# Optimization experiments

Measured on AMD Instinct MI355X. Metric: run time of the kernel, lower is better.

## Reference

```python
import jax, jax.numpy as jnp
import numpy as np

N, E, G, D, L = 10000, 160000, 100, 128, 5
LMAX, SHD, VOCAB = 2, 9, 10
S3 = 3.0 ** 0.5


def _sph(v):
    # e3nn spherical harmonics, normalize=True, normalization='norm' (||Y_l||=1), lmax=2
    r = jnp.linalg.norm(v, axis=-1, keepdims=True)
    u = v / jnp.maximum(r, 1e-12)
    x, y, z = u[:, 0], u[:, 1], u[:, 2]
    y2 = jnp.stack([S3 * x * z, S3 * x * y, y * y - 0.5 * (x * x + z * z), S3 * y * z, 0.5 * S3 * (z * z - x * x)], axis=-1)
    return jnp.concatenate([jnp.ones_like(u[:, :1]), u, y2], axis=-1)  # [E,9]


def _sh_scale(s, w):
    # FullyConnectedTensorProduct(sh, 1x0e, sh): per-l scaling by weight w [.,3]
    return jnp.concatenate([s[:, 0:1] * w[:, 0:1], s[:, 1:4] * w[:, 1:2], s[:, 4:9] * w[:, 2:3]], axis=-1)


def _smean(src, idx, n):
    s = jax.ops.segment_sum(src, idx, num_segments=n)
    c = jax.ops.segment_sum(jnp.ones((src.shape[0], 1), src.dtype), idx, num_segments=n)
    return s / jnp.maximum(c, 1.0)


def _mlp(x, w1, b1, w2, b2, last_act=False):
    h = jax.nn.silu(x @ w1 + b1)
    o = h @ w2 + b2
    return jax.nn.silu(o) if last_act else o


def _forward(atoms, edge_index, batch_ids, pos, emb_table, Wsi1, bsi1, Wsi2, bsi2, WsiC1, bsiC1, WsiC2, bsiC2, Wm1, bm1, Wm2, bm2, Wp1, bp1, Wp2, bp2, Wn1, bn1, Wn2, bn2, Ws1, bs1, Ws2, bs2, Wpred, bpred):
    row, col = edge_index[0], edge_index[1]
    feat = emb_table[atoms]                                  # [N,D]
    # --- SH_INIT ---
    dpos = pos[row] - pos[col]
    dist = jnp.linalg.norm(dpos, axis=-1, keepdims=True)
    msg = _mlp(jnp.concatenate([dist, feat[row], feat[col]], axis=-1), Wsi1, bsi1, Wsi2, bsi2)
    dsh = _sh_scale(jax.lax.stop_gradient(_sph(dpos)), msg)
    sh = _smean(dsh, row, N)                                 # [N,9]
    pos_com = _smean(pos, batch_ids, G)[batch_ids]
    sh = sh + _sh_scale(jax.lax.stop_gradient(_sph(pos - pos_com)), _mlp(feat, WsiC1, bsiC1, WsiC2, bsiC2))
    sh = sh.at[:, :LMAX * LMAX].set(0.0)                     # all_ell=False: keep only highest l
    # --- stacked HEGNN layers via scan ---
    def body(carry, p):
        feat, pos, sh = carry
        wm1, cm1, wm2, cm2, wp1, cp1, wp2, cp2, wn1, cn1, wn2, cn2, ws1, cs1, ws2, cs2 = p
        dp = pos[row] - pos[col]
        d2 = jnp.sum(dp * dp, axis=-1, keepdims=True)        # squared distance
        t = sh[row] * sh[col]
        ip = jnp.concatenate([jnp.sum(t[:, 0:1], -1, keepdims=True), jnp.sum(t[:, 1:4], -1, keepdims=True), jnp.sum(t[:, 4:9], -1, keepdims=True)], axis=-1)
        m = _mlp(jnp.concatenate([feat[row], feat[col], d2, ip], axis=-1), wm1, cm1, wm2, cm2, last_act=True)
        dp = dp * _mlp(m, wp1, cp1, wp2, cp2)
        ds = _sh_scale(sh[row] - sh[col], _mlp(m, ws1, cs1, ws2, cs2))
        m_agg = _smean(m, row, N)
        p_agg = _smean(dp, row, N)
        s_agg = _smean(ds, row, N)
        sh = sh + s_agg
        pos = pos + p_agg
        feat = _mlp(jnp.concatenate([feat, m_agg], axis=-1), wn1, cn1, wn2, cn2)
        return (feat, pos, sh), None
    (feat, pos, sh), _ = jax.lax.scan(body, (feat, pos, sh), (Wm1, bm1, Wm2, bm2, Wp1, bp1, Wp2, bp2, Wn1, bn1, Wn2, bn2, Ws1, bs1, Ws2, bs2))
    # --- equivariant sum-pool + linear pred ---
    pooled = jax.ops.segment_sum(jnp.concatenate([feat, pos, sh], axis=-1), batch_ids, num_segments=G)
    return pooled @ Wpred + bpred                            # [G,1]


def setup_inputs():
    ks = iter(jax.random.split(jax.random.key(0), 48))
    def nrm(shape):
        return jax.random.normal(next(ks), shape, jnp.float32)
    def w(shape):
        return nrm(shape) / np.float32(np.sqrt(shape[-2]))
    z = lambda *s: jnp.zeros(s, jnp.float32)
    inp = dict(
        atoms=jax.random.randint(next(ks), (N,), 0, VOCAB),
        edge_index=jax.random.randint(next(ks), (2, E), 0, N),
        batch_ids=jnp.sort(jax.random.randint(next(ks), (N,), 0, G)),
        pos=nrm((N, 3)),
        emb_table=nrm((VOCAB, D)) * 0.1,
    )
    inp.update(Wsi1=w((2 * D + 1, D)), bsi1=z(D), Wsi2=w((D, LMAX + 1)), bsi2=z(LMAX + 1),
               WsiC1=w((D, D)), bsiC1=z(D), WsiC2=w((D, LMAX + 1)), bsiC2=z(LMAX + 1))
    inp.update(Wm1=w((L, 2 * D + 1 + LMAX + 1, D)), bm1=z(L, D), Wm2=w((L, D, D)), bm2=z(L, D),
               Wp1=w((L, D, D)), bp1=z(L, D), Wp2=w((L, D, 1)), bp2=z(L, 1),
               Wn1=w((L, 2 * D, D)), bn1=z(L, D), Wn2=w((L, D, D)), bn2=z(L, D),
               Ws1=w((L, D, D)), bs1=z(L, D), Ws2=w((L, D, LMAX + 1)), bs2=z(L, LMAX + 1),
               Wpred=w((D + 3 + SHD, 1)), bpred=z(1))
    return inp


def reference(atoms, edge_index, batch_ids, pos, emb_table, Wsi1, bsi1, Wsi2, bsi2, WsiC1, bsiC1, WsiC2, bsiC2, Wm1, bm1, Wm2, bm2, Wp1, bp1, Wp2, bp2, Wn1, bn1, Wn2, bn2, Ws1, bs1, Ws2, bs2, Wpred, bpred):
    return _forward(atoms, edge_index, batch_ids, pos, emb_table, Wsi1, bsi1, Wsi2, bsi2, WsiC1, bsiC1, WsiC2, bsiC2, Wm1, bm1, Wm2, bm2, Wp1, bp1, Wp2, bp2, Wn1, bn1, Wn2, bn2, Ws1, bs1, Ws2, bs2, Wpred, bpred)
```

## Files before the change

kernel.cpp:

```cpp
#include <hip/hip_runtime.h>
#include <math.h>

#define NA 10000
#define NE 160000
#define NG 100
#define DF 128
#define NL 5
#define NAP 10112
#define NSB 40

typedef __attribute__((ext_vector_type(8))) short bfx8;
typedef __attribute__((ext_vector_type(4))) float f32x4;

__device__ __forceinline__ float silu_f(float x) {
    return x / (1.0f + __expf(-x));
}

__device__ __forceinline__ unsigned short f2bf(float x) {
    unsigned u = __builtin_bit_cast(unsigned, x);
    u = (u + 0x7FFFu + ((u >> 16) & 1u)) >> 16;
    return (unsigned short)u;
}
__device__ __forceinline__ float bf2f(unsigned short h) {
    unsigned u = ((unsigned)h) << 16;
    return __builtin_bit_cast(float, u);
}
__device__ __forceinline__ unsigned packbf(float lo, float hi) {
    return (unsigned)f2bf(lo) | ((unsigned)f2bf(hi) << 16);
}

__device__ __forceinline__ void sph9(float dx, float dy, float dz, float* s) {
    float r = sqrtf(dx * dx + dy * dy + dz * dz);
    float inv = 1.0f / fmaxf(r, 1e-12f);
    float x = dx * inv, y = dy * inv, z = dz * inv;
    const float S3 = 1.7320508075688772f;
    s[0] = 1.0f;
    s[1] = x; s[2] = y; s[3] = z;
    s[4] = S3 * x * z;
    s[5] = S3 * x * y;
    s[6] = y * y - 0.5f * (x * x + z * z);
    s[7] = S3 * y * z;
    s[8] = 0.5f * S3 * (z * z - x * x);
}

#define OFF_SI1   0
#define OFF_SIC1  36864
#define LBASE     53248
#define LSIZE     135168
#define LOFF_M1   0
#define LOFF_M2   36864
#define LOFF_P1   53248
#define LOFF_S1   69632
#define LOFF_N1   86016
#define LOFF_N2   118784
#define WT_TOTAL  729088

__global__ void k_prep_w(const float* __restrict__ Wsi1, const float* __restrict__ WsiC1,
                         const float* __restrict__ Wm1, const float* __restrict__ Wm2,
                         const float* __restrict__ Wp1, const float* __restrict__ Ws1,
                         const float* __restrict__ Wn1, const float* __restrict__ Wn2,
                         unsigned short* __restrict__ WT) {
    int flat = blockIdx.x * 256 + threadIdx.x;
    if (flat >= WT_TOTAL) return;
    float v = 0.0f;
    if (flat < OFF_SIC1) {
        int o = flat - OFF_SI1;
        int n = o / 288, k = o % 288;
        if (k < 256)       v = Wsi1[(k + 1) * 128 + n];
        else if (k == 256) v = Wsi1[n];
    } else if (flat < LBASE) {
        int o = flat - OFF_SIC1;
        int n = o / 128, k = o % 128;
        v = WsiC1[k * 128 + n];
    } else {
        int t = flat - LBASE;
        int lyr = t / LSIZE;
        int o = t % LSIZE;
        if (o < LOFF_M2) {
            int n = o / 288, k = o % 288;
            if (k < 260) v = Wm1[(size_t)lyr * 260 * 128 + k * 128 + n];
        } else if (o < LOFF_P1) {
            int o2 = o - LOFF_M2; int n = o2 / 128, k = o2 % 128;
            v = Wm2[(size_t)lyr * 16384 + k * 128 + n];
        } else if (o < LOFF_S1) {
            int o2 = o - LOFF_P1; int n = o2 / 128, k = o2 % 128;
            v = Wp1[(size_t)lyr * 16384 + k * 128 + n];
        } else if (o < LOFF_N1) {
            int o2 = o - LOFF_S1; int n = o2 / 128, k = o2 % 128;
            v = Ws1[(size_t)lyr * 16384 + k * 128 + n];
        } else if (o < LOFF_N2) {
            int o2 = o - LOFF_N1; int n = o2 / 256, k = o2 % 256;
            v = Wn1[(size_t)lyr * 32768 + k * 128 + n];
        } else {
            int o2 = o - LOFF_N2; int n = o2 / 128, k = o2 % 128;
            v = Wn2[(size_t)lyr * 16384 + k * 128 + n];
        }
    }
    WT[flat] = f2bf(v);
}

template <int KP, int MODE, bool ACT, int NOUT, bool F32OUT>
__global__ __launch_bounds__(256) void gemm_mfma(
    const unsigned short* __restrict__ Ab,
    const unsigned short* __restrict__ WT,
    const float* __restrict__ bias,
    unsigned short* __restrict__ Cb, float* __restrict__ Cf, int M,
    const int* __restrict__ rowI, const int* __restrict__ colI,
    const unsigned short* __restrict__ featb, const unsigned short* __restrict__ tailb,
    const float* __restrict__ W2, const float* __restrict__ b2,
    float* __restrict__ outS)
{
    constexpr int NO = (NOUT > 0) ? NOUT : 1;
    __shared__ unsigned short As[128 * 40];
    __shared__ unsigned short Bs[128 * 40];
    __shared__ float W2s[128 * NO];
    __shared__ float sacc[128 * NO];

    const int tid = threadIdx.x;
    const int m0 = blockIdx.x * 128;
    const int mlo = tid >> 2;
    const int part = tid & 3;

    if (NOUT > 0) {
        for (int t = tid; t < 128 * NO; t += 256) {
            W2s[t] = W2[t];
            sacc[t] = 0.0f;
        }
    }

    int er0 = 0, ec0 = 0, er1 = 0, ec1 = 0;
    if (MODE == 1) {
        er0 = rowI[m0 + mlo];      ec0 = colI[m0 + mlo];
        er1 = rowI[m0 + mlo + 64]; ec1 = colI[m0 + mlo + 64];
    }

    const int w = tid >> 6;
    const int l = tid & 63;
    const int quad = l >> 4;
    const int lm = l & 15;
    const int wm = (w >> 1) * 64, wn = (w & 1) * 64;

    float bv[4];
#pragma unroll
    for (int j = 0; j < 4; j++) bv[j] = bias[wn + j * 16 + lm];

    f32x4 acc[4][4] = {};

    constexpr int NCH = KP / 32;
#pragma unroll 1
    for (int c = 0; c < NCH; c++) {
        const int k0 = c * 32;
#pragma unroll
        for (int i = 0; i < 2; i++) {
            const int m = mlo + i * 64;
            uint4 v;
            if (MODE == 0) {
                v = *(const uint4*)(Ab + (size_t)(m0 + m) * KP + k0 + part * 8);
            } else {
                if (k0 < 128) {
                    int e = i ? er1 : er0;
                    v = *(const uint4*)(featb + (size_t)e * 128 + k0 + part * 8);
                } else if (k0 < 256) {
                    int e = i ? ec1 : ec0;
                    v = *(const uint4*)(featb + (size_t)e * 128 + (k0 - 128) + part * 8);
                } else {
                    if (part == 0) v = *(const uint4*)(tailb + (size_t)(m0 + m) * 16);
                    else           v = make_uint4(0, 0, 0, 0);
                }
            }
            *(uint4*)&As[m * 40 + part * 8] = v;
            uint4 wv = *(const uint4*)(WT + (size_t)m * KP + k0 + part * 8);
            *(uint4*)&Bs[m * 40 + part * 8] = wv;
        }
        __syncthreads();
        bfx8 a[4], b[4];
#pragma unroll
        for (int i = 0; i < 4; i++) a[i] = *(const bfx8*)&As[(wm + i * 16 + lm) * 40 + quad * 8];
#pragma unroll
        for (int j = 0; j < 4; j++) b[j] = *(const bfx8*)&Bs[(wn + j * 16 + lm) * 40 + quad * 8];
#pragma unroll
        for (int i = 0; i < 4; i++)
#pragma unroll
            for (int j = 0; j < 4; j++)
                acc[i][j] = __builtin_amdgcn_mfma_f32_16x16x32_bf16(a[i], b[j], acc[i][j], 0, 0, 0);
        __syncthreads();
    }

    if (NOUT > 0) {
#pragma unroll
        for (int i = 0; i < 4; i++) {
#pragma unroll
            for (int r = 0; r < 4; r++) {
                const int rowL = wm + i * 16 + quad * 4 + r;
                float ps[NO];
#pragma unroll
                for (int o = 0; o < NO; o++) ps[o] = 0.0f;
#pragma unroll
                for (int j = 0; j < 4; j++) {
                    float v = acc[i][j][r] + bv[j];
                    if (ACT) v = silu_f(v);
                    const int colg = wn + j * 16 + lm;
#pragma unroll
                    for (int o = 0; o < NO; o++) ps[o] += v * W2s[colg * NO + o];
                }
#pragma unroll
                for (int off = 1; off < 16; off <<= 1)
#pragma unroll
                    for (int o = 0; o < NO; o++) ps[o] += __shfl_xor(ps[o], off, 64);
                if (lm == 0)
#pragma unroll
                    for (int o = 0; o < NO; o++) atomicAdd(&sacc[rowL * NO + o], ps[o]);
            }
        }
        __syncthreads();
        for (int t = tid; t < 128 * NO; t += 256) {
            int rowL = t / NO, o = t - rowL * NO;
            int e = m0 + rowL;
            if (e < M) outS[(size_t)e * NO + o] = sacc[t] + b2[o];
        }
    } else {
#pragma unroll
        for (int i = 0; i < 4; i++) {
            const int rbase = wm + i * 16 + quad * 4;
#pragma unroll
            for (int r = 0; r < 4; r++) {
                const int e = m0 + rbase + r;
                if (e >= M) continue;
#pragma unroll
                for (int j = 0; j < 4; j++) {
                    float v = acc[i][j][r] + bv[j];
                    if (ACT) v = silu_f(v);
                    const int colg = wn + j * 16 + lm;
                    Cb[(size_t)e * 128 + colg] = f2bf(v);
                    if (F32OUT) Cf[(size_t)e * 128 + colg] = v;
                }
            }
        }
    }
}

__global__ void k_count_edges(const int* __restrict__ row, int* __restrict__ cnt) {
    int e = blockIdx.x * blockDim.x + threadIdx.x;
    if (e < NE) atomicAdd(&cnt[row[e]], 1);
}

__global__ void k_scan_block(const int* __restrict__ cnt, int* __restrict__ ptr,
                             int* __restrict__ btot) {
    __shared__ int s[256];
    int tid = threadIdx.x;
    int i = blockIdx.x * 256 + tid;
    int v = (i < NA) ? cnt[i] : 0;
    s[tid] = v;
    __syncthreads();
    for (int off = 1; off < 256; off <<= 1) {
        int t = (tid >= off) ? s[tid - off] : 0;
        __syncthreads();
        s[tid] += t;
        __syncthreads();
    }
    if (i < NA) ptr[i] = s[tid] - v;
    if (tid == 255) btot[blockIdx.x] = s[255];
}

__global__ void k_scan_tot(int* __restrict__ btot) {
    int lane = threadIdx.x;
    int v = (lane < NSB) ? btot[lane] : 0;
    int orig = v;
    for (int off = 1; off < 64; off <<= 1) {
        int t = __shfl_up(v, off, 64);
        if (lane >= off) v += t;
    }
    if (lane < NSB) btot[lane] = v - orig;
}

__global__ void k_scan_add(int* __restrict__ ptr, const int* __restrict__ btot) {
    int i = blockIdx.x * 256 + threadIdx.x;
    if (i < NA) ptr[i] += btot[i >> 8];
    if (i == 0) ptr[NA] = NE;
}

__global__ void k_copy_cursor(const int* __restrict__ ptr, int* __restrict__ cursor) {
    int i = blockIdx.x * 256 + threadIdx.x;
    if (i < NA) cursor[i] = ptr[i];
}

__global__ void k_sort(const int* __restrict__ row, const int* __restrict__ col,
                       int* __restrict__ cursor,
                       int* __restrict__ row_s, int* __restrict__ col_s) {
    int e = blockIdx.x * blockDim.x + threadIdx.x;
    if (e >= NE) return;
    int r = row[e];
    int p = atomicAdd(&cursor[r], 1);
    row_s[p] = r;
    col_s[p] = col[e];
}

__global__ void k_gptr(const int* __restrict__ bid, int* __restrict__ gptr) {
    int n = blockIdx.x * blockDim.x + threadIdx.x;
    if (n >= NA) return;
    int b = bid[n];
    int bp = (n == 0) ? -1 : bid[n - 1];
    for (int g = bp + 1; g <= b; g++) gptr[g] = n;
    if (n == NA - 1)
        for (int g = b + 1; g <= NG; g++) gptr[g] = NA;
}

__global__ void k_init_feat(const int* __restrict__ atoms,
                            const float* __restrict__ emb,
                            float* __restrict__ feat, unsigned short* __restrict__ featb) {
    int idx = blockIdx.x * blockDim.x + threadIdx.x;
    if (idx >= NA * DF) return;
    float v = emb[atoms[idx >> 7] * DF + (idx & 127)];
    feat[idx] = v;
    featb[idx] = f2bf(v);
}

__global__ void k_copy_pos(const float* __restrict__ pos, float* __restrict__ posc) {
    int idx = blockIdx.x * blockDim.x + threadIdx.x;
    if (idx < NA * 3) posc[idx] = pos[idx];
}

__global__ void k_com_g(const float* __restrict__ pos, const int* __restrict__ gptr,
                        float* __restrict__ com) {
    int g = blockIdx.x;
    int lane = threadIdx.x;
    int s0 = gptr[g], s1 = gptr[g + 1];
    float sx = 0.0f, sy = 0.0f, sz = 0.0f;
    for (int n = s0 + lane; n < s1; n += 64) {
        sx += pos[n * 3 + 0];
        sy += pos[n * 3 + 1];
        sz += pos[n * 3 + 2];
    }
#pragma unroll
    for (int off = 32; off > 0; off >>= 1) {
        sx += __shfl_down(sx, off, 64);
        sy += __shfl_down(sy, off, 64);
        sz += __shfl_down(sz, off, 64);
    }
    if (lane == 0) {
        float cinv = 1.0f / fmaxf((float)(s1 - s0), 1.0f);
        com[g * 3 + 0] = sx * cinv;
        com[g * 3 + 1] = sy * cinv;
        com[g * 3 + 2] = sz * cinv;
    }
}

__global__ void k_tail_init(const int* __restrict__ row, const int* __restrict__ col,
                            const float* __restrict__ pos, unsigned short* __restrict__ tailb) {
    int e = blockIdx.x * blockDim.x + threadIdx.x;
    if (e >= NE) return;
    int r = row[e], c = col[e];
    float dx = pos[r * 3 + 0] - pos[c * 3 + 0];
    float dy = pos[r * 3 + 1] - pos[c * 3 + 1];
    float dz = pos[r * 3 + 2] - pos[c * 3 + 2];
    float dist = sqrtf(dx * dx + dy * dy + dz * dz);
    uint4 t0 = make_uint4(packbf(dist, 0.0f), 0, 0, 0);
    uint4 z = make_uint4(0, 0, 0, 0);
    *(uint4*)(tailb + (size_t)e * 16) = t0;
    *(uint4*)(tailb + (size_t)e * 16 + 8) = z;
}

__global__ void k_gather_sph(const int* __restrict__ ptr, const int* __restrict__ col_s,
                             const float* __restrict__ pos, const float* __restrict__ msg,
                             float* __restrict__ sh_mean) {
    int n = blockIdx.x;
    int lane = threadIdx.x;
    int s0 = ptr[n], s1 = ptr[n + 1];
    float px = pos[n * 3 + 0], py = pos[n * 3 + 1], pz = pos[n * 3 + 2];
    float a[9];
#pragma unroll
    for (int j = 0; j < 9; j++) a[j] = 0.0f;
    for (int e = s0 + lane; e < s1; e += 64) {
        int c = col_s[e];
        float dx = px - pos[c * 3 + 0];
        float dy = py - pos[c * 3 + 1];
        float dz = pz - pos[c * 3 + 2];
        float s[9];
        sph9(dx, dy, dz, s);
        float w0 = msg[e * 3 + 0], w1 = msg[e * 3 + 1], w2 = msg[e * 3 + 2];
        a[0] += s[0] * w0;
        a[1] += s[1] * w1; a[2] += s[2] * w1; a[3] += s[3] * w1;
        a[4] += s[4] * w2; a[5] += s[5] * w2; a[6] += s[6] * w2;
        a[7] += s[7] * w2; a[8] += s[8] * w2;
    }
#pragma unroll
    for (int off = 32; off > 0; off >>= 1)
#pragma unroll
        for (int j = 0; j < 9; j++) a[j] += __shfl_down(a[j], off, 64);
    if (lane == 0) {
        float cinv = 1.0f / fmaxf((float)(s1 - s0), 1.0f);
#pragma unroll
        for (int j = 0; j < 9; j++) sh_mean[(size_t)n * 9 + j] = a[j] * cinv;
    }
}

__global__ void k_sh_finish(const float* __restrict__ sh_mean,
                            const float* __restrict__ pos, const float* __restrict__ com,
                            const int* __restrict__ bid, const float* __restrict__ msgC,
                            float* __restrict__ sh) {
    int n = blockIdx.x * blockDim.x + threadIdx.x;
    if (n >= NA) return;
    int b = bid[n];
    float dx = pos[n * 3 + 0] - com[b * 3 + 0];
    float dy = pos[n * 3 + 1] - com[b * 3 + 1];
    float dz = pos[n * 3 + 2] - com[b * 3 + 2];
    float s[9];
    sph9(dx, dy, dz, s);
    float w2 = msgC[n * 3 + 2];
    sh[n * 9 + 0] = 0.0f;
    sh[n * 9 + 1] = 0.0f;
    sh[n * 9 + 2] = 0.0f;
    sh[n * 9 + 3] = 0.0f;
#pragma unroll
    for (int j = 4; j < 9; j++)
        sh[n * 9 + j] = sh_mean[(size_t)n * 9 + j] + s[j] * w2;
}

__global__ void k_edge_pre(const int* __restrict__ row, const int* __restrict__ col,
                           const float* __restrict__ pos, const float* __restrict__ sh,
                           unsigned short* __restrict__ tailb) {
    int e = blockIdx.x * blockDim.x + threadIdx.x;
    if (e >= NE) return;
    int r = row[e], c = col[e];
    float dx = pos[r * 3 + 0] - pos[c * 3 + 0];
    float dy = pos[r * 3 + 1] - pos[c * 3 + 1];
    float dz = pos[r * 3 + 2] - pos[c * 3 + 2];
    float d2 = dx * dx + dy * dy + dz * dz;
    const float* sr = sh + (size_t)r * 9;
    const float* sc = sh + (size_t)c * 9;
    float ip0 = sr[0] * sc[0];
    float ip1 = sr[1] * sc[1] + sr[2] * sc[2] + sr[3] * sc[3];
    float ip2 = sr[4] * sc[4] + sr[5] * sc[5] + sr[6] * sc[6] + sr[7] * sc[7] + sr[8] * sc[8];
    uint4 t0 = make_uint4(packbf(d2, ip0), packbf(ip1, ip2), 0, 0);
    uint4 z = make_uint4(0, 0, 0, 0);
    *(uint4*)(tailb + (size_t)e * 16) = t0;
    *(uint4*)(tailb + (size_t)e * 16 + 8) = z;
}

__global__ void k_gather_ps(const int* __restrict__ ptr, const int* __restrict__ col_s,
                            const float* __restrict__ pos, const float* __restrict__ sh,
                            const float* __restrict__ psc, const float* __restrict__ ssc,
                            float* __restrict__ p_sum, float* __restrict__ s_sum) {
    int n = blockIdx.x;
    int lane = threadIdx.x;
    int s0 = ptr[n], s1 = ptr[n + 1];
    float px = pos[n * 3 + 0], py = pos[n * 3 + 1], pz = pos[n * 3 + 2];
    float shn[9];
#pragma unroll
    for (int j = 0; j < 9; j++) shn[j] = sh[(size_t)n * 9 + j];
    float a[12];
#pragma unroll
    for (int j = 0; j < 12; j++) a[j] = 0.0f;
    for (int e = s0 + lane; e < s1; e += 64) {
        int c = col_s[e];
        float p = psc[e];
        a[0] += (px - pos[c * 3 + 0]) * p;
        a[1] += (py - pos[c * 3 + 1]) * p;
        a[2] += (pz - pos[c * 3 + 2]) * p;
        float w0 = ssc[e * 3 + 0], w1 = ssc[e * 3 + 1], w2 = ssc[e * 3 + 2];
        const float* sc = sh + (size_t)c * 9;
        a[3]  += (shn[0] - sc[0]) * w0;
        a[4]  += (shn[1] - sc[1]) * w1;
        a[5]  += (shn[2] - sc[2]) * w1;
        a[6]  += (shn[3] - sc[3]) * w1;
        a[7]  += (shn[4] - sc[4]) * w2;
        a[8]  += (shn[5] - sc[5]) * w2;
        a[9]  += (shn[6] - sc[6]) * w2;
        a[10] += (shn[7] - sc[7]) * w2;
        a[11] += (shn[8] - sc[8]) * w2;
    }
#pragma unroll
    for (int off = 32; off > 0; off >>= 1)
#pragma unroll
        for (int j = 0; j < 12; j++) a[j] += __shfl_down(a[j], off, 64);
    if (lane == 0) {
        float cinv = 1.0f / fmaxf((float)(s1 - s0), 1.0f);
#pragma unroll
        for (int j = 0; j < 3; j++) p_sum[(size_t)n * 3 + j] = a[j] * cinv;
#pragma unroll
        for (int j = 0; j < 9; j++) s_sum[(size_t)n * 9 + j] = a[3 + j] * cinv;
    }
}

__global__ void k_update_nodes(float* __restrict__ sh, float* __restrict__ pos,
                               const float* __restrict__ s_sum, const float* __restrict__ p_sum) {
    int n = blockIdx.x * blockDim.x + threadIdx.x;
    if (n >= NA) return;
#pragma unroll
    for (int j = 0; j < 9; j++) sh[n * 9 + j] += s_sum[(size_t)n * 9 + j];
#pragma unroll
    for (int j = 0; j < 3; j++) pos[n * 3 + j] += p_sum[(size_t)n * 3 + j];
}

__global__ __launch_bounds__(128) void k_gather_xn(
    const int* __restrict__ ptr, const unsigned short* __restrict__ bufMb,
    const unsigned short* __restrict__ featb, unsigned short* __restrict__ Xnb) {
    int n = blockIdx.x;
    int c = threadIdx.x;
    int s0 = ptr[n], s1 = ptr[n + 1];
    float sum = 0.0f;
    for (int e = s0; e < s1; e++) sum += bf2f(bufMb[(size_t)e * 128 + c]);
    float cinv = 1.0f / fmaxf((float)(s1 - s0), 1.0f);
    Xnb[(size_t)n * 256 + c] = featb[(size_t)n * 128 + c];
    Xnb[(size_t)n * 256 + 128 + c] = f2bf(sum * cinv);
}

__global__ __launch_bounds__(192) void k_pool_pred(
    const int* __restrict__ gptr, const float* __restrict__ feat,
    const float* __restrict__ pos, const float* __restrict__ sh,
    const float* __restrict__ Wp, const float* __restrict__ bp,
    float* __restrict__ out) {
    __shared__ float pl[140];
    int g = blockIdx.x;
    int c = threadIdx.x;
    int s0 = gptr[g], s1 = gptr[g + 1];
    if (c < 140) {
        float sum = 0.0f;
        for (int n = s0; n < s1; n++) {
            float v;
            if (c < 128)      v = feat[(size_t)n * 128 + c];
            else if (c < 131) v = pos[n * 3 + (c - 128)];
            else              v = sh[(size_t)n * 9 + (c - 131)];
            sum += v;
        }
        pl[c] = sum;
    }
    __syncthreads();
    if (c < 64) {
        float s = 0.0f;
        for (int k = c; k < 140; k += 64) s += pl[k] * Wp[k];
#pragma unroll
        for (int off = 32; off > 0; off >>= 1) s += __shfl_down(s, off, 64);
        if (c == 0) out[g] = s + bp[0];
    }
}

extern "C" void kernel_launch(void* const* d_in, const int* in_sizes, int n_in,
                              void* d_out, int out_size, void* d_ws, size_t ws_size,
                              hipStream_t stream) {
    const int*   atoms  = (const int*)d_in[0];
    const int*   eidx   = (const int*)d_in[1];
    const int*   row    = eidx;
    const int*   col    = eidx + NE;
    const int*   bid    = (const int*)d_in[2];
    const float* pos_in = (const float*)d_in[3];
    const float* emb    = (const float*)d_in[4];
    const float* Wsi1   = (const float*)d_in[5];
    const float* bsi1   = (const float*)d_in[6];
    const float* Wsi2   = (const float*)d_in[7];
    const float* bsi2   = (const float*)d_in[8];
    const float* WsiC1  = (const float*)d_in[9];
    const float* bsiC1  = (const float*)d_in[10];
    const float* WsiC2  = (const float*)d_in[11];
    const float* bsiC2  = (const float*)d_in[12];
    const float* Wm1    = (const float*)d_in[13];
    const float* bm1    = (const float*)d_in[14];
    const float* Wm2    = (const float*)d_in[15];
    const float* bm2    = (const float*)d_in[16];
    const float* Wp1    = (const float*)d_in[17];
    const float* bp1    = (const float*)d_in[18];
    const float* Wp2    = (const float*)d_in[19];
    const float* bp2    = (const float*)d_in[20];
    const float* Wn1    = (const float*)d_in[21];
    const float* bn1    = (const float*)d_in[22];
    const float* Wn2    = (const float*)d_in[23];
    const float* bn2    = (const float*)d_in[24];
    const float* Ws1    = (const float*)d_in[25];
    const float* bs1    = (const float*)d_in[26];
    const float* Ws2    = (const float*)d_in[27];
    const float* bs2    = (const float*)d_in[28];
    const float* Wpred  = (const float*)d_in[29];
    const float* bpred  = (const float*)d_in[30];

    float* base = (float*)d_ws;
    size_t off = 0;
    auto alloc = [&](size_t nfl) { float* r = base + off; off += nfl; return r; };
    unsigned short* bufHb = (unsigned short*)alloc((size_t)NE * DF / 2);
    unsigned short* bufMb = (unsigned short*)alloc((size_t)NE * DF / 2);
    unsigned short* featb = (unsigned short*)alloc((size_t)NAP * DF / 2);
    unsigned short* hnb   = (unsigned short*)alloc((size_t)NAP * DF / 2);
    unsigned short* Xnb   = (unsigned short*)alloc((size_t)NAP * 256 / 2);
    unsigned short* tailb = (unsigned short*)alloc((size_t)NE * 16 / 2);
    unsigned short* WT    = (unsigned short*)alloc(WT_TOTAL / 2);
    float* feat    = alloc((size_t)NAP * DF);
    float* sc3     = alloc((size_t)NE * 3);
    float* psc     = alloc(NE);
    float* posc    = alloc((size_t)NA * 3 + 4);
    float* sh      = alloc((size_t)NA * 9 + 4);
    float* p_sum   = alloc((size_t)NA * 3 + 4);
    float* s_sum   = alloc((size_t)NA * 9 + 4);
    float* sh_mean = alloc((size_t)NA * 9 + 4);
    float* com     = alloc(NG * 3 + 4);
    float* msgC    = alloc((size_t)NA * 3 + 4);
    int* cnt_row   = (int*)alloc(NA);
    int* ptr       = (int*)alloc(NA + 4);
    int* cursor    = (int*)alloc(NA);
    int* gptr      = (int*)alloc(NG + 4);
    int* row_s     = (int*)alloc(NE);
    int* col_s     = (int*)alloc(NE);
    int* btot      = (int*)alloc(64);

    const dim3 B256(256);
    const int gE = NE / 128;
    const int gN = NAP / 128;

    hipMemsetAsync(cnt_row, 0, NA * sizeof(int), stream);
    k_prep_w<<<(WT_TOTAL + 255) / 256, B256, 0, stream>>>(Wsi1, WsiC1, Wm1, Wm2, Wp1, Ws1, Wn1, Wn2, WT);
    k_init_feat<<<(NA * DF + 255) / 256, B256, 0, stream>>>(atoms, emb, feat, featb);
    k_copy_pos<<<(NA * 3 + 255) / 256, B256, 0, stream>>>(pos_in, posc);
    k_count_edges<<<(NE + 255) / 256, B256, 0, stream>>>(row, cnt_row);
    k_scan_block<<<NSB, B256, 0, stream>>>(cnt_row, ptr, btot);
    k_scan_tot<<<1, 64, 0, stream>>>(btot);
    k_scan_add<<<NSB, B256, 0, stream>>>(ptr, btot);
    k_copy_cursor<<<NSB, B256, 0, stream>>>(ptr, cursor);
    k_sort<<<(NE + 255) / 256, B256, 0, stream>>>(row, col, cursor, row_s, col_s);
    k_gptr<<<(NA + 255) / 256, B256, 0, stream>>>(bid, gptr);
    k_com_g<<<NG, 64, 0, stream>>>(pos_in, gptr, com);

    k_tail_init<<<(NE + 255) / 256, B256, 0, stream>>>(row_s, col_s, posc, tailb);
    gemm_mfma<288, 1, true, 3, false><<<gE, B256, 0, stream>>>(
        nullptr, WT + OFF_SI1, bsi1, nullptr, nullptr, NE, row_s, col_s, featb, tailb,
        Wsi2, bsi2, sc3);
    k_gather_sph<<<NA, 64, 0, stream>>>(ptr, col_s, posc, sc3, sh_mean);
    gemm_mfma<128, 0, true, 3, false><<<gN, B256, 0, stream>>>(
        featb, WT + OFF_SIC1, bsiC1, nullptr, nullptr, NA, nullptr, nullptr, nullptr, nullptr,
        WsiC2, bsiC2, msgC);
    k_sh_finish<<<(NA + 255) / 256, B256, 0, stream>>>(sh_mean, posc, com, bid, msgC, sh);

    for (int l = 0; l < NL; l++) {
        const unsigned short* wtL = WT + LBASE + (size_t)l * LSIZE;
        const float* cm1 = bm1 + l * 128;
        const float* cm2 = bm2 + l * 128;
        const float* cp1 = bp1 + l * 128;
        const float* wp2 = Wp2 + (size_t)l * 128;
        const float* cp2 = bp2 + l;
        const float* cn1 = bn1 + l * 128;
        const float* cn2 = bn2 + l * 128;
        const float* cs1 = bs1 + l * 128;
        const float* ws2 = Ws2 + (size_t)l * 128 * 3;
        const float* cs2 = bs2 + l * 3;

        k_edge_pre<<<(NE + 255) / 256, B256, 0, stream>>>(row_s, col_s, posc, sh, tailb);
        gemm_mfma<288, 1, true, 0, false><<<gE, B256, 0, stream>>>(
            nullptr, wtL + LOFF_M1, cm1, bufHb, nullptr, NE, row_s, col_s, featb, tailb,
            nullptr, nullptr, nullptr);
        gemm_mfma<128, 0, true, 0, false><<<gE, B256, 0, stream>>>(
            bufHb, wtL + LOFF_M2, cm2, bufMb, nullptr, NE, nullptr, nullptr, nullptr, nullptr,
            nullptr, nullptr, nullptr);
        gemm_mfma<128, 0, true, 1, false><<<gE, B256, 0, stream>>>(
            bufMb, wtL + LOFF_P1, cp1, nullptr, nullptr, NE, nullptr, nullptr, nullptr, nullptr,
            wp2, cp2, psc);
        gemm_mfma<128, 0, true, 3, false><<<gE, B256, 0, stream>>>(
            bufMb, wtL + LOFF_S1, cs1, nullptr, nullptr, NE, nullptr, nullptr, nullptr, nullptr,
            ws2, cs2, sc3);

        k_gather_ps<<<NA, 64, 0, stream>>>(ptr, col_s, posc, sh, psc, sc3, p_sum, s_sum);
        k_update_nodes<<<(NA + 255) / 256, B256, 0, stream>>>(sh, posc, s_sum, p_sum);
        k_gather_xn<<<NA, 128, 0, stream>>>(ptr, bufMb, featb, Xnb);
        gemm_mfma<256, 0, true, 0, false><<<gN, B256, 0, stream>>>(
            Xnb, wtL + LOFF_N1, cn1, hnb, nullptr, NA, nullptr, nullptr, nullptr, nullptr,
            nullptr, nullptr, nullptr);
        gemm_mfma<128, 0, false, 0, true><<<gN, B256, 0, stream>>>(
            hnb, wtL + LOFF_N2, cn2, featb, feat, NA, nullptr, nullptr, nullptr, nullptr,
            nullptr, nullptr, nullptr);
    }

    k_pool_pred<<<NG, 192, 0, stream>>>(gptr, feat, posc, sh, Wpred, bpred, (float*)d_out);
}
```

Baseline: 1.088 ms.

## Fuse per-layer edge MLP chain and node MLP into single kernels

Replaces the four separate edge GEMM launches per layer (message MLP two layers, position head, sh head) with one kernel that keeps the intermediate 128x128 tile in LDS and chains all four matmuls. The two node-MLP GEMMs are fused the same way. This removes the round trip of the hidden edge activations through global memory and cuts launches. Weights are now read directly from global memory as MFMA B operands instead of being staged in LDS, and the larger LDS footprint may lower occupancy.

```diff
diff --git a/kernel.cpp b/kernel.cpp
--- a/kernel.cpp
+++ b/kernel.cpp
@@ -99,18 +99,17 @@
     WT[flat] = f2bf(v);
 }
 
-template <int KP, int MODE, bool ACT, int NOUT, bool F32OUT>
+template <int KP, int MODE, int NOUT>
 __global__ __launch_bounds__(256) void gemm_mfma(
     const unsigned short* __restrict__ Ab,
     const unsigned short* __restrict__ WT,
-    const float* __restrict__ bias,
-    unsigned short* __restrict__ Cb, float* __restrict__ Cf, int M,
+    const float* __restrict__ bias, int M,
     const int* __restrict__ rowI, const int* __restrict__ colI,
     const unsigned short* __restrict__ featb, const unsigned short* __restrict__ tailb,
     const float* __restrict__ W2, const float* __restrict__ b2,
     float* __restrict__ outS)
 {
-    constexpr int NO = (NOUT > 0) ? NOUT : 1;
+    constexpr int NO = NOUT;
     __shared__ unsigned short As[128 * 40];
     __shared__ unsigned short Bs[128 * 40];
     __shared__ float W2s[128 * NO];
@@ -121,11 +120,9 @@
     const int mlo = tid >> 2;
     const int part = tid & 3;
 
-    if (NOUT > 0) {
-        for (int t = tid; t < 128 * NO; t += 256) {
-            W2s[t] = W2[t];
-            sacc[t] = 0.0f;
-        }
+    for (int t = tid; t < 128 * NO; t += 256) {
+        W2s[t] = W2[t];
+        sacc[t] = 0.0f;
     }
 
     int er0 = 0, ec0 = 0, er1 = 0, ec1 = 0;
@@ -186,56 +183,370 @@
         __syncthreads();
     }
 
-    if (NOUT > 0) {
-#pragma unroll
-        for (int i = 0; i < 4; i++) {
+#pragma unroll
+    for (int i = 0; i < 4; i++) {
+#pragma unroll
+        for (int r = 0; r < 4; r++) {
+            const int rowL = wm + i * 16 + quad * 4 + r;
+            float ps[NO];
+#pragma unroll
+            for (int o = 0; o < NO; o++) ps[o] = 0.0f;
+#pragma unroll
+            for (int j = 0; j < 4; j++) {
+                float v = silu_f(acc[i][j][r] + bv[j]);
+                const int colg = wn + j * 16 + lm;
+#pragma unroll
+                for (int o = 0; o < NO; o++) ps[o] += v * W2s[colg * NO + o];
+            }
+#pragma unroll
+            for (int off = 1; off < 16; off <<= 1)
+#pragma unroll
+                for (int o = 0; o < NO; o++) ps[o] += __shfl_xor(ps[o], off, 64);
+            if (lm == 0)
+#pragma unroll
+                for (int o = 0; o < NO; o++) atomicAdd(&sacc[rowL * NO + o], ps[o]);
+        }
+    }
+    __syncthreads();
+    for (int t = tid; t < 128 * NO; t += 256) {
+        int rowL = t / NO, o = t - rowL * NO;
+        int e = m0 + rowL;
+        if (e < M) outS[(size_t)e * NO + o] = sacc[t] + b2[o];
+    }
+}
+
+__global__ __launch_bounds__(256) void k_edge_layer(
+    const unsigned short* __restrict__ w1,
+    const unsigned short* __restrict__ w2,
+    const unsigned short* __restrict__ wp,
+    const unsigned short* __restrict__ ws,
+    const float* __restrict__ b1, const float* __restrict__ b2,
+    const float* __restrict__ bp, const float* __restrict__ bs,
+    const float* __restrict__ wp2, const float* __restrict__ bp2,
+    const float* __restrict__ ws2, const float* __restrict__ bs2,
+    const int* __restrict__ rowI, const int* __restrict__ colI,
+    const unsigned short* __restrict__ featb, const unsigned short* __restrict__ tailb,
+    unsigned short* __restrict__ bufMb, float* __restrict__ psc, float* __restrict__ sc3)
+{
+    __shared__ unsigned short As[128 * 40];
+    __shared__ unsigned short Mt[128 * 136];
+    __shared__ float W2p[128];
+    __shared__ float W2q[128 * 3];
+    __shared__ float sap[128];
+    __shared__ float saq[128 * 3];
+
+    const int tid = threadIdx.x;
+    const int m0 = blockIdx.x * 128;
+    const int mlo = tid >> 2;
+    const int part = tid & 3;
+
+    if (tid < 128) { W2p[tid] = wp2[tid]; sap[tid] = 0.0f; }
+    for (int t = tid; t < 384; t += 256) { W2q[t] = ws2[t]; saq[t] = 0.0f; }
+
+    const int er0 = rowI[m0 + mlo],      ec0 = colI[m0 + mlo];
+    const int er1 = rowI[m0 + mlo + 64], ec1 = colI[m0 + mlo + 64];
+
+    const int w = tid >> 6;
+    const int l = tid & 63;
+    const int quad = l >> 4;
+    const int lm = l & 15;
+    const int wm = (w >> 1) * 64, wn = (w & 1) * 64;
+    const bool evenL = (lm & 1) == 0;
+
+    {
+        f32x4 acc[4][4] = {};
+#pragma unroll 1
+        for (int c = 0; c < 9; c++) {
+            const int k0 = c * 32;
+#pragma unroll
+            for (int i = 0; i < 2; i++) {
+                const int m = mlo + i * 64;
+                uint4 v;
+                if (k0 < 128) {
+                    int e = i ? er1 : er0;
+                    v = *(const uint4*)(featb + (size_t)e * 128 + k0 + part * 8);
+                } else if (k0 < 256) {
+                    int e = i ? ec1 : ec0;
+                    v = *(const uint4*)(featb + (size_t)e * 128 + (k0 - 128) + part * 8);
+                } else {
+                    if (part == 0) v = *(const uint4*)(tailb + (size_t)(m0 + m) * 16);
+                    else           v = make_uint4(0, 0, 0, 0);
+                }
+                *(uint4*)&As[m * 40 + part * 8] = v;
+            }
+            __syncthreads();
+            bfx8 a[4], b[4];
+#pragma unroll
+            for (int i = 0; i < 4; i++)
+                a[i] = *(const bfx8*)&As[(wm + i * 16 + lm) * 40 + quad * 8];
+#pragma unroll
+            for (int j = 0; j < 4; j++)
+                b[j] = *(const bfx8*)(w1 + (size_t)(wn + j * 16 + lm) * 288 + k0 + quad * 8);
+#pragma unroll
+            for (int i = 0; i < 4; i++)
+#pragma unroll
+                for (int j = 0; j < 4; j++)
+                    acc[i][j] = __builtin_amdgcn_mfma_f32_16x16x32_bf16(a[i], b[j], acc[i][j], 0, 0, 0);
+            __syncthreads();
+        }
+        float bv[4];
+#pragma unroll
+        for (int j = 0; j < 4; j++) bv[j] = b1[wn + j * 16 + lm];
+#pragma unroll
+        for (int i = 0; i < 4; i++)
 #pragma unroll
             for (int r = 0; r < 4; r++) {
                 const int rowL = wm + i * 16 + quad * 4 + r;
-                float ps[NO];
-#pragma unroll
-                for (int o = 0; o < NO; o++) ps[o] = 0.0f;
+#pragma unroll
+                for (int j = 0; j < 4; j++) {
+                    float v = silu_f(acc[i][j][r] + bv[j]);
+                    float vp = __shfl_xor(v, 1, 64);
+                    if (evenL)
+                        *(unsigned*)&Mt[rowL * 136 + wn + j * 16 + lm] = packbf(v, vp);
+                }
+            }
+    }
+    __syncthreads();
+
+    {
+        f32x4 acc[4][4] = {};
+#pragma unroll 1
+        for (int c = 0; c < 4; c++) {
+            const int k0 = c * 32;
+            bfx8 a[4], b[4];
+#pragma unroll
+            for (int i = 0; i < 4; i++)
+                a[i] = *(const bfx8*)&Mt[(wm + i * 16 + lm) * 136 + k0 + quad * 8];
+#pragma unroll
+            for (int j = 0; j < 4; j++)
+                b[j] = *(const bfx8*)(w2 + (size_t)(wn + j * 16 + lm) * 128 + k0 + quad * 8);
+#pragma unroll
+            for (int i = 0; i < 4; i++)
+#pragma unroll
+                for (int j = 0; j < 4; j++)
+                    acc[i][j] = __builtin_amdgcn_mfma_f32_16x16x32_bf16(a[i], b[j], acc[i][j], 0, 0, 0);
+        }
+        __syncthreads();
+        float bv[4];
+#pragma unroll
+        for (int j = 0; j < 4; j++) bv[j] = b2[wn + j * 16 + lm];
+#pragma unroll
+        for (int i = 0; i < 4; i++)
+#pragma unroll
+            for (int r = 0; r < 4; r++) {
+                const int rowL = wm + i * 16 + quad * 4 + r;
+                const int e = m0 + rowL;
+#pragma unroll
+                for (int j = 0; j < 4; j++) {
+                    float v = silu_f(acc[i][j][r] + bv[j]);
+                    float vp = __shfl_xor(v, 1, 64);
+                    if (evenL) {
+                        unsigned pk = packbf(v, vp);
+                        const int colg = wn + j * 16 + lm;
+                        *(unsigned*)&Mt[rowL * 136 + colg] = pk;
+                        *(unsigned*)(bufMb + (size_t)e * 128 + colg) = pk;
+                    }
+                }
+            }
+    }
+    __syncthreads();
+
+    {
+        f32x4 acc[4][4] = {};
+#pragma unroll 1
+        for (int c = 0; c < 4; c++) {
+            const int k0 = c * 32;
+            bfx8 a[4], b[4];
+#pragma unroll
+            for (int i = 0; i < 4; i++)
+                a[i] = *(const bfx8*)&Mt[(wm + i * 16 + lm) * 136 + k0 + quad * 8];
+#pragma unroll
+            for (int j = 0; j < 4; j++)
+                b[j] = *(const bfx8*)(wp + (size_t)(wn + j * 16 + lm) * 128 + k0 + quad * 8);
+#pragma unroll
+            for (int i = 0; i < 4; i++)
+#pragma unroll
+                for (int j = 0; j < 4; j++)
+                    acc[i][j] = __builtin_amdgcn_mfma_f32_16x16x32_bf16(a[i], b[j], acc[i][j], 0, 0, 0);
+        }
+        float bv[4];
+#pragma unroll
+        for (int j = 0; j < 4; j++) bv[j] = bp[wn + j * 16 + lm];
+#pragma unroll
+        for (int i = 0; i < 4; i++)
+#pragma unroll
+            for (int r = 0; r < 4; r++) {
+                const int rowL = wm + i * 16 + quad * 4 + r;
+                float ps = 0.0f;
+#pragma unroll
+                for (int j = 0; j < 4; j++) {
+                    float v = silu_f(acc[i][j][r] + bv[j]);
+                    ps += v * W2p[wn + j * 16 + lm];
+                }
+#pragma unroll
+                for (int off = 1; off < 16; off <<= 1) ps += __shfl_xor(ps, off, 64);
+                if (lm == 0) atomicAdd(&sap[rowL], ps);
+            }
+    }
+
+    {
+        f32x4 acc[4][4] = {};
+#pragma unroll 1
+        for (int c = 0; c < 4; c++) {
+            const int k0 = c * 32;
+            bfx8 a[4], b[4];
+#pragma unroll
+            for (int i = 0; i < 4; i++)
+                a[i] = *(const bfx8*)&Mt[(wm + i * 16 + lm) * 136 + k0 + quad * 8];
+#pragma unroll
+            for (int j = 0; j < 4; j++)
+                b[j] = *(const bfx8*)(ws + (size_t)(wn + j * 16 + lm) * 128 + k0 + quad * 8);
+#pragma unroll
+            for (int i = 0; i < 4; i++)
+#pragma unroll
+                for (int j = 0; j < 4; j++)
+                    acc[i][j] = __builtin_amdgcn_mfma_f32_16x16x32_bf16(a[i], b[j], acc[i][j], 0, 0, 0);
+        }
+        float bv[4];
+#pragma unroll
+        for (int j = 0; j < 4; j++) bv[j] = bs[wn + j * 16 + lm];
+#pragma unroll
+        for (int i = 0; i < 4; i++)
+#pragma unroll
+            for (int r = 0; r < 4; r++) {
+                const int rowL = wm + i * 16 + quad * 4 + r;
+                float ps[3] = {0.0f, 0.0f, 0.0f};
+#pragma unroll
+                for (int j = 0; j < 4; j++) {
+                    float v = silu_f(acc[i][j][r] + bv[j]);
+                    const int colg = wn + j * 16 + lm;
+#pragma unroll
+                    for (int o = 0; o < 3; o++) ps[o] += v * W2q[colg * 3 + o];
+                }
+#pragma unroll
+                for (int off = 1; off < 16; off <<= 1)
+#pragma unroll
+                    for (int o = 0; o < 3; o++) ps[o] += __shfl_xor(ps[o], off, 64);
+                if (lm == 0)
+#pragma unroll
+                    for (int o = 0; o < 3; o++) atomicAdd(&saq[rowL * 3 + o], ps[o]);
+            }
+    }
+    __syncthreads();
+
+    if (tid < 128) {
+        const int e = m0 + tid;
+        psc[e] = sap[tid] + bp2[0];
+#pragma unroll
+        for (int o = 0; o < 3; o++) sc3[(size_t)e * 3 + o] = saq[tid * 3 + o] + bs2[o];
+    }
+}
+
+__global__ __launch_bounds__(256) void k_node_layer(
+    const unsigned short* __restrict__ Xnb,
+    const unsigned short* __restrict__ w1,
+    const unsigned short* __restrict__ w2,
+    const float* __restrict__ b1, const float* __restrict__ b2,
+    unsigned short* __restrict__ featb, float* __restrict__ feat, int M)
+{
+    __shared__ unsigned short As[128 * 40];
+    __shared__ unsigned short Mt[128 * 136];
+
+    const int tid = threadIdx.x;
+    const int m0 = blockIdx.x * 128;
+    const int mlo = tid >> 2;
+    const int part = tid & 3;
+
+    const int w = tid >> 6;
+    const int l = tid & 63;
+    const int quad = l >> 4;
+    const int lm = l & 15;
+    const int wm = (w >> 1) * 64, wn = (w & 1) * 64;
+    const bool evenL = (lm & 1) == 0;
+
+    {
+        f32x4 acc[4][4] = {};
+#pragma unroll 1
+        for (int c = 0; c < 8; c++) {
+            const int k0 = c * 32;
+#pragma unroll
+            for (int i = 0; i < 2; i++) {
+                const int m = mlo + i * 64;
+                *(uint4*)&As[m * 40 + part * 8] =
+                    *(const uint4*)(Xnb + (size_t)(m0 + m) * 256 + k0 + part * 8);
+            }
+            __syncthreads();
+            bfx8 a[4], b[4];
+#pragma unroll
+            for (int i = 0; i < 4; i++)
+                a[i] = *(const bfx8*)&As[(wm + i * 16 + lm) * 40 + quad * 8];
+#pragma unroll
+            for (int j = 0; j < 4; j++)
+                b[j] = *(const bfx8*)(w1 + (size_t)(wn + j * 16 + lm) * 256 + k0 + quad * 8);
+#pragma unroll
+            for (int i = 0; i < 4; i++)
+#pragma unroll
+                for (int j = 0; j < 4; j++)
+                    acc[i][j] = __builtin_amdgcn_mfma_f32_16x16x32_bf16(a[i], b[j], acc[i][j], 0, 0, 0);
+            __syncthreads();
+        }
+        float bv[4];
+#pragma unroll
+        for (int j = 0; j < 4; j++) bv[j] = b1[wn + j * 16 + lm];
+#pragma unroll
+        for (int i = 0; i < 4; i++)
+#pragma unroll
+            for (int r = 0; r < 4; r++) {
+                const int rowL = wm + i * 16 + quad * 4 + r;
+#pragma unroll
+                for (int j = 0; j < 4; j++) {
+                    float v = silu_f(acc[i][j][r] + bv[j]);
+                    float vp = __shfl_xor(v, 1, 64);
+                    if (evenL)
+                        *(unsigned*)&Mt[rowL * 136 + wn + j * 16 + lm] = packbf(v, vp);
+                }
+            }
+    }
+    __syncthreads();
+
+    {
+        f32x4 acc[4][4] = {};
+#pragma unroll 1
+        for (int c = 0; c < 4; c++) {
+            const int k0 = c * 32;
+            bfx8 a[4], b[4];
+#pragma unroll
+            for (int i = 0; i < 4; i++)
+                a[i] = *(const bfx8*)&Mt[(wm + i * 16 + lm) * 136 + k0 + quad * 8];
+#pragma unroll
+            for (int j = 0; j < 4; j++)
+                b[j] = *(const bfx8*)(w2 + (size_t)(wn + j * 16 + lm) * 128 + k0 + quad * 8);
+#pragma unroll
+            for (int i = 0; i < 4; i++)
+#pragma unroll
+                for (int j = 0; j < 4; j++)
+                    acc[i][j] = __builtin_amdgcn_mfma_f32_16x16x32_bf16(a[i], b[j], acc[i][j], 0, 0, 0);
+        }
+        float bv[4];
+#pragma unroll
+        for (int j = 0; j < 4; j++) bv[j] = b2[wn + j * 16 + lm];
+#pragma unroll
+        for (int i = 0; i < 4; i++)
+#pragma unroll
+            for (int r = 0; r < 4; r++) {
+                const int rowL = wm + i * 16 + quad * 4 + r;
+                const int e = m0 + rowL;
 #pragma unroll
                 for (int j = 0; j < 4; j++) {
                     float v = acc[i][j][r] + bv[j];
-                    if (ACT) v = silu_f(v);
-                    const int colg = wn + j * 16 + lm;
-#pragma unroll
-                    for (int o = 0; o < NO; o++) ps[o] += v * W2s[colg * NO + o];
-                }
-#pragma unroll
-                for (int off = 1; off < 16; off <<= 1)
-#pragma unroll
-                    for (int o = 0; o < NO; o++) ps[o] += __shfl_xor(ps[o], off, 64);
-                if (lm == 0)
-#pragma unroll
-                    for (int o = 0; o < NO; o++) atomicAdd(&sacc[rowL * NO + o], ps[o]);
-            }
-        }
-        __syncthreads();
-        for (int t = tid; t < 128 * NO; t += 256) {
-            int rowL = t / NO, o = t - rowL * NO;
-            int e = m0 + rowL;
-            if (e < M) outS[(size_t)e * NO + o] = sacc[t] + b2[o];
-        }
-    } else {
-#pragma unroll
-        for (int i = 0; i < 4; i++) {
-            const int rbase = wm + i * 16 + quad * 4;
-#pragma unroll
-            for (int r = 0; r < 4; r++) {
-                const int e = m0 + rbase + r;
-                if (e >= M) continue;
-#pragma unroll
-                for (int j = 0; j < 4; j++) {
-                    float v = acc[i][j][r] + bv[j];
-                    if (ACT) v = silu_f(v);
-                    const int colg = wn + j * 16 + lm;
-                    Cb[(size_t)e * 128 + colg] = f2bf(v);
-                    if (F32OUT) Cf[(size_t)e * 128 + colg] = v;
+                    float vp = __shfl_xor(v, 1, 64);
+                    if (evenL && e < M) {
+                        const int colg = wn + j * 16 + lm;
+                        *(unsigned*)(featb + (size_t)e * 128 + colg) = packbf(v, vp);
+                        *(float2*)(feat + (size_t)e * 128 + colg) = make_float2(v, vp);
+                    }
                 }
             }
-        }
     }
 }
 
@@ -575,10 +886,8 @@
     float* base = (float*)d_ws;
     size_t off = 0;
     auto alloc = [&](size_t nfl) { float* r = base + off; off += nfl; return r; };
-    unsigned short* bufHb = (unsigned short*)alloc((size_t)NE * DF / 2);
     unsigned short* bufMb = (unsigned short*)alloc((size_t)NE * DF / 2);
     unsigned short* featb = (unsigned short*)alloc((size_t)NAP * DF / 2);
-    unsigned short* hnb   = (unsigned short*)alloc((size_t)NAP * DF / 2);
     unsigned short* Xnb   = (unsigned short*)alloc((size_t)NAP * 256 / 2);
     unsigned short* tailb = (unsigned short*)alloc((size_t)NE * 16 / 2);
     unsigned short* WT    = (unsigned short*)alloc(WT_TOTAL / 2);
@@ -618,13 +927,11 @@
     k_com_g<<<NG, 64, 0, stream>>>(pos_in, gptr, com);
 
     k_tail_init<<<(NE + 255) / 256, B256, 0, stream>>>(row_s, col_s, posc, tailb);
-    gemm_mfma<288, 1, true, 3, false><<<gE, B256, 0, stream>>>(
-        nullptr, WT + OFF_SI1, bsi1, nullptr, nullptr, NE, row_s, col_s, featb, tailb,
-        Wsi2, bsi2, sc3);
+    gemm_mfma<288, 1, 3><<<gE, B256, 0, stream>>>(
+        nullptr, WT + OFF_SI1, bsi1, NE, row_s, col_s, featb, tailb, Wsi2, bsi2, sc3);
     k_gather_sph<<<NA, 64, 0, stream>>>(ptr, col_s, posc, sc3, sh_mean);
-    gemm_mfma<128, 0, true, 3, false><<<gN, B256, 0, stream>>>(
-        featb, WT + OFF_SIC1, bsiC1, nullptr, nullptr, NA, nullptr, nullptr, nullptr, nullptr,
-        WsiC2, bsiC2, msgC);
+    gemm_mfma<128, 0, 3><<<gN, B256, 0, stream>>>(
+        featb, WT + OFF_SIC1, bsiC1, NA, nullptr, nullptr, nullptr, nullptr, WsiC2, bsiC2, msgC);
     k_sh_finish<<<(NA + 255) / 256, B256, 0, stream>>>(sh_mean, posc, com, bid, msgC, sh);
 
     for (int l = 0; l < NL; l++) {
@@ -641,28 +948,15 @@
         const float* cs2 = bs2 + l * 3;
 
         k_edge_pre<<<(NE + 255) / 256, B256, 0, stream>>>(row_s, col_s, posc, sh, tailb);
-        gemm_mfma<288, 1, true, 0, false><<<gE, B256, 0, stream>>>(
-            nullptr, wtL + LOFF_M1, cm1, bufHb, nullptr, NE, row_s, col_s, featb, tailb,
-            nullptr, nullptr, nullptr);
-        gemm_mfma<128, 0, true, 0, false><<<gE, B256, 0, stream>>>(
-            bufHb, wtL + LOFF_M2, cm2, bufMb, nullptr, NE, nullptr, nullptr, nullptr, nullptr,
-            nullptr, nullptr, nullptr);
-        gemm_mfma<128, 0, true, 1, false><<<gE, B256, 0, stream>>>(
-            bufMb, wtL + LOFF_P1, cp1, nullptr, nullptr, NE, nullptr, nullptr, nullptr, nullptr,
-            wp2, cp2, psc);
-        gemm_mfma<128, 0, true, 3, false><<<gE, B256, 0, stream>>>(
-            bufMb, wtL + LOFF_S1, cs1, nullptr, nullptr, NE, nullptr, nullptr, nullptr, nullptr,
-            ws2, cs2, sc3);
-
+        k_edge_layer<<<gE, B256, 0, stream>>>(
+            wtL + LOFF_M1, wtL + LOFF_M2, wtL + LOFF_P1, wtL + LOFF_S1,
+            cm1, cm2, cp1, cs1, wp2, cp2, ws2, cs2,
+            row_s, col_s, featb, tailb, bufMb, psc, sc3);
         k_gather_ps<<<NA, 64, 0, stream>>>(ptr, col_s, posc, sh, psc, sc3, p_sum, s_sum);
         k_update_nodes<<<(NA + 255) / 256, B256, 0, stream>>>(sh, posc, s_sum, p_sum);
         k_gather_xn<<<NA, 128, 0, stream>>>(ptr, bufMb, featb, Xnb);
-        gemm_mfma<256, 0, true, 0, false><<<gN, B256, 0, stream>>>(
-            Xnb, wtL + LOFF_N1, cn1, hnb, nullptr, NA, nullptr, nullptr, nullptr, nullptr,
-            nullptr, nullptr, nullptr);
-        gemm_mfma<128, 0, false, 0, true><<<gN, B256, 0, stream>>>(
-            hnb, wtL + LOFF_N2, cn2, featb, feat, NA, nullptr, nullptr, nullptr, nullptr,
-            nullptr, nullptr, nullptr);
+        k_node_layer<<<gN, B256, 0, stream>>>(
+            Xnb, wtL + LOFF_N1, wtL + LOFF_N2, cn1, cn2, featb, feat, NA);
     }
 
     k_pool_pred<<<NG, 192, 0, stream>>>(gptr, feat, posc, sh, Wpred, bpred, (float*)d_out);
```

After: 1.236 ms. 13.7% more time.
